# Kernel optimization log

Hardware: AMD Instinct MI355X
Metric: run time of the kernel (lower is better)

The kernel has to match this reference:

```python
import jax, jax.numpy as jnp
import numpy as np

N_NODES = 50000
N_EDGES = 800000
NFEAT = 128
NHID = 128
NCLASS = 10
NUM_GRAPHS = 512


def setup_inputs() -> dict:
    key = jax.random.key(0)
    ks = jax.random.split(key, 12)
    x = jax.random.normal(ks[0], (N_NODES, NFEAT), dtype=jnp.float32)
    edge_index = jax.random.randint(ks[1], (2, N_EDGES), 0, N_NODES, dtype=jnp.int64)
    batch = jnp.sort(jax.random.randint(ks[2], (N_NODES,), 0, NUM_GRAPHS, dtype=jnp.int64))
    def glorot(k, fan_in, fan_out):
        lim = np.sqrt(6.0 / (fan_in + fan_out))
        return jax.random.uniform(k, (fan_in, fan_out), jnp.float32, -lim, lim)
    return {
        "x": x, "edge_index": edge_index, "batch": batch,
        "W0": glorot(ks[3], NFEAT, NHID), "b0": jnp.zeros((NHID,), jnp.float32),
        "W1": glorot(ks[4], NHID, NHID), "b1": jnp.zeros((NHID,), jnp.float32),
        "W2": glorot(ks[5], NHID, NHID), "b2": jnp.zeros((NHID,), jnp.float32),
        "lin_w": glorot(ks[6], NHID, NCLASS), "lin_b": jnp.zeros((NCLASS,), jnp.float32),
    }


def _gcn_norm(edge_index, n):
    # PyG GCNConv: add self-loops, symmetric normalization D^-1/2 A D^-1/2
    loop = jnp.arange(n, dtype=edge_index.dtype)
    src = jnp.concatenate([edge_index[0], loop])  # [E+N]
    dst = jnp.concatenate([edge_index[1], loop])
    deg = jax.ops.segment_sum(jnp.ones_like(dst, dtype=jnp.float32), dst, num_segments=n)
    dis = jnp.where(deg > 0, jax.lax.rsqrt(jnp.maximum(deg, 1.0)), 0.0)
    norm = dis[src] * dis[dst]  # [E+N]
    return src, dst, norm


def _gcn_conv(x, W, b, src, dst, norm, n):
    h = x @ W                              # [N, nhid]
    msg = h[src] * norm[:, None]           # gather + scale, [E+N, nhid]
    out = jax.ops.segment_sum(msg, dst, num_segments=n)
    return out + b


def reference(x, edge_index, batch, W0, b0, W1, b1, W2, b2, lin_w, lin_b):
    n = x.shape[0]
    src, dst, norm = _gcn_norm(edge_index, n)
    h = x
    for (W, b) in ((W0, b0), (W1, b1), (W2, b2)):
        h = jax.nn.relu(_gcn_conv(h, W, b, src, dst, norm, n))
    # global mean pool over graphs
    sums = jax.ops.segment_sum(h, batch, num_segments=NUM_GRAPHS)
    cnts = jax.ops.segment_sum(jnp.ones((n,), jnp.float32), batch, num_segments=NUM_GRAPHS)
    pooled = sums / jnp.maximum(cnts, 1.0)[:, None]  # [G, nhid]
    logits = pooled @ lin_w + lin_b
    return jax.nn.log_softmax(logits, axis=-1)
```

## Files before the change

### kernel.cpp

```cpp
#include <hip/hip_runtime.h>
#include <hip/hip_fp16.h>


#define FEAT 128
#define NCLASS 10
#define NB_MAX 512

typedef _Float16 h8 __attribute__((ext_vector_type(8)));
typedef float f4 __attribute__((ext_vector_type(4)));

__device__ inline int swz(int row, int cbyte) { return row * 256 + (cbyte ^ ((row & 7) << 4)); }

__global__ void __launch_bounds__(256) hist_wt_kernel(const int* __restrict__ ei,
                                                      int* __restrict__ bhist,
                                                      int ne, int nb, int epb, int hb,
                                                      const float* __restrict__ W0,
                                                      const float* __restrict__ W1,
                                                      const float* __restrict__ W2,
                                                      _Float16* __restrict__ Wt) {
  int t = threadIdx.x;
  if (blockIdx.x >= hb) {
    int i = (blockIdx.x - hb) * 256 + t;
    if (i < 3 * FEAT * FEAT) {
      int l = i / (FEAT * FEAT);
      int r = i - l * (FEAT * FEAT);
      int nn = r >> 7, kk = r & 127;
      const float* W = (l == 0) ? W0 : (l == 1) ? W1 : W2;
      Wt[i] = (_Float16)W[kk * FEAT + nn];
    }
    return;
  }
  __shared__ int lh[NB_MAX];
  for (int i = t; i < nb; i += 256) lh[i] = 0;
  __syncthreads();
  int r0 = blockIdx.x * epb;
  int r1 = min(r0 + epb, ne);
  for (int k = r0 + t; k < r1; k += 256) atomicAdd(&lh[ei[ne + k] >> 7], 1);
  __syncthreads();
  for (int i = t; i < nb; i += 256)
    if (lh[i]) atomicAdd(&bhist[i], lh[i]);
}

__global__ void __launch_bounds__(512) bscan_kernel(const int* __restrict__ bhist,
                                                    int* __restrict__ bstart,
                                                    int* __restrict__ bcur,
                                                    int* __restrict__ off,
                                                    int nb, int n, int ne) {
  __shared__ int sh[512];
  int t = threadIdx.x;
  int v = (t < nb) ? bhist[t] : 0;
  sh[t] = v;
  __syncthreads();
  int x = v;
  for (int d = 1; d < 512; d <<= 1) {
    int y = (t >= d) ? sh[t - d] : 0;
    __syncthreads();
    x += y;
    sh[t] = x;
    __syncthreads();
  }
  if (t < nb) {
    bstart[t] = x - v;
    bcur[t] = x - v;
  }
  if (t == 0) {
    bstart[nb] = ne;
    off[n] = ne;
  }
}

__global__ void __launch_bounds__(256) scatter_kernel(const int* __restrict__ ei,
                                                      int* __restrict__ bcur,
                                                      unsigned* __restrict__ buf,
                                                      int ne, int nb, int epb) {
  __shared__ int lh[NB_MAX], lbs[NB_MAX];
  int t = threadIdx.x;
  for (int i = t; i < nb; i += 256) lh[i] = 0;
  __syncthreads();
  int r0 = blockIdx.x * epb;
  int r1 = min(r0 + epb, ne);
  for (int k = r0 + t; k < r1; k += 256) atomicAdd(&lh[ei[ne + k] >> 7], 1);
  __syncthreads();
  for (int i = t; i < nb; i += 256) {
    int c = lh[i];
    lbs[i] = c ? atomicAdd(&bcur[i], c) : 0;
    lh[i] = 0;
  }
  __syncthreads();
  for (int k = r0 + t; k < r1; k += 256) {
    int src = ei[k];
    int dst = ei[ne + k];
    int b = dst >> 7;
    int p = lbs[b] + atomicAdd(&lh[b], 1);
    buf[p] = (unsigned)src | ((unsigned)(dst & 127) << 25);
  }
}

__global__ void __launch_bounds__(256) bucket_build_kernel(const unsigned* __restrict__ buf,
                                                           const int* __restrict__ bstart,
                                                           int* __restrict__ off,
                                                           int* __restrict__ csr,
                                                           float* __restrict__ dis, int n) {
  __shared__ int cnt[128], cur[128], sh[128];
  int b = blockIdx.x, t = threadIdx.x;
  int e0 = bstart[b], e1 = bstart[b + 1];
  if (t < 128) cnt[t] = 0;
  __syncthreads();
  for (int k = e0 + t; k < e1; k += 256) atomicAdd(&cnt[buf[k] >> 25], 1);
  __syncthreads();
  int v = (t < 128) ? cnt[t] : 0;
  if (t < 128) sh[t] = v;
  __syncthreads();
  int x = v;
  for (int d = 1; d < 128; d <<= 1) {
    int y = (t < 128 && t >= d) ? sh[t - d] : 0;
    __syncthreads();
    if (t < 128) {
      x += y;
      sh[t] = x;
    }
    __syncthreads();
  }
  if (t < 128) {
    int node = (b << 7) + t;
    cur[t] = x - v;
    if (node < n) {
      off[node] = e0 + x - v;
      dis[node] = rsqrtf((float)(v + 1));
    }
  }
  __syncthreads();
  for (int k = e0 + t; k < e1; k += 256) {
    unsigned u = buf[k];
    int d = u >> 25;
    int p = atomicAdd(&cur[d], 1);
    csr[e0 + p] = (int)(u & 0x1FFFFFFu);
  }
}

template <bool F32IN>
__global__ void __launch_bounds__(256) gemm_mfma_kernel(const void* __restrict__ Xin,
                                                        const _Float16* __restrict__ Wt,
                                                        const float* __restrict__ dis,
                                                        _Float16* __restrict__ Hs, int n) {
  __shared__ _Float16 st[64 * FEAT];
  int tid = threadIdx.x;
  int w = tid >> 6, lane = tid & 63;
  int l15 = lane & 15, hi = lane >> 4;

  int rowA = blockIdx.x * 64 + w * 16 + l15;
  int rA = min(rowA, n - 1);
  const _Float16* Xh = (const _Float16*)Xin;
  const float* Xf = (const float*)Xin;

  f4 acc[8];
#pragma unroll
  for (int nb = 0; nb < 8; ++nb) acc[nb] = (f4)(0.f);

#pragma unroll
  for (int kk = 0; kk < FEAT; kk += 32) {
    int ko = kk + hi * 8;
    h8 a;
    if (F32IN) {
      float4 x0 = *(const float4*)&Xf[(size_t)rA * FEAT + ko];
      float4 x1 = *(const float4*)&Xf[(size_t)rA * FEAT + ko + 4];
      a[0] = (_Float16)x0.x; a[1] = (_Float16)x0.y; a[2] = (_Float16)x0.z; a[3] = (_Float16)x0.w;
      a[4] = (_Float16)x1.x; a[5] = (_Float16)x1.y; a[6] = (_Float16)x1.z; a[7] = (_Float16)x1.w;
    } else {
      a = *(const h8*)&Xh[(size_t)rA * FEAT + ko];
    }
#pragma unroll
    for (int nb = 0; nb < 8; ++nb) {
      h8 bfr = *(const h8*)&Wt[(nb * 16 + l15) * FEAT + ko];
      acc[nb] = __builtin_amdgcn_mfma_f32_16x16x32_f16(a, bfr, acc[nb], 0, 0, 0);
    }
  }

  float dv[4];
#pragma unroll
  for (int r = 0; r < 4; ++r) {
    int grow = blockIdx.x * 64 + w * 16 + hi * 4 + r;
    dv[r] = dis[min(grow, n - 1)];
  }
#pragma unroll
  for (int nb = 0; nb < 8; ++nb)
#pragma unroll
    for (int r = 0; r < 4; ++r)
      st[(w * 16 + hi * 4 + r) * FEAT + nb * 16 + l15] = (_Float16)(acc[nb][r] * dv[r]);
  __syncthreads();

  int rowbase = blockIdx.x * 64;
#pragma unroll
  for (int i = tid; i < 64 * FEAT / 8; i += 256) {
    int row = rowbase + (i >> 4);
    if (row < n)
      *(uint4*)&Hs[(size_t)row * FEAT + (i & 15) * 8] =
          *(const uint4*)&st[(i >> 4) * FEAT + (i & 15) * 8];
  }
}

__global__ void __launch_bounds__(256) fused_kernel(const h8* __restrict__ Hs_in,
                                                    const int* __restrict__ csr,
                                                    const int* __restrict__ off,
                                                    const float* __restrict__ dis,
                                                    const float* __restrict__ bias,
                                                    const _Float16* __restrict__ Wt,
                                                    _Float16* __restrict__ Hs_out, int n) {
  __shared__ char xsb[64 * 256];
  int tid = threadIdx.x;
  int w = tid >> 6, lane = tid & 63;
  int grp = lane >> 4, lig = lane & 15;
  int row0 = blockIdx.x * 64;
  int g16 = w * 4 + grp;

  float4 b0 = ((const float4*)bias)[lig * 2];
  float4 b1 = ((const float4*)bias)[lig * 2 + 1];
  float bb[8] = {b0.x, b0.y, b0.z, b0.w, b1.x, b1.y, b1.z, b1.w};

  for (int m = 0; m < 4; ++m) {
    int ar = g16 * 4 + m;
    int nd = min(row0 + ar, n - 1);
    int s = off[nd], e = off[nd + 1];
    float a0[8], a1[8], a2[8], a3[8];
    h8 v = Hs_in[(size_t)nd * 16 + lig];
#pragma unroll
    for (int j = 0; j < 8; ++j) {
      a0[j] = (float)v[j];
      a1[j] = a2[j] = a3[j] = 0.f;
    }
    for (int k = s; k < e; k += 4) {
      int i0 = csr[k];
      int i1 = (k + 1 < e) ? csr[k + 1] : -1;
      int i2 = (k + 2 < e) ? csr[k + 2] : -1;
      int i3 = (k + 3 < e) ? csr[k + 3] : -1;
      h8 v0 = Hs_in[(size_t)i0 * 16 + lig];
      h8 v1 = Hs_in[(size_t)max(i1, 0) * 16 + lig];
      h8 v2 = Hs_in[(size_t)max(i2, 0) * 16 + lig];
      h8 v3 = Hs_in[(size_t)max(i3, 0) * 16 + lig];
#pragma unroll
      for (int j = 0; j < 8; ++j) a0[j] += (float)v0[j];
      if (i1 >= 0) {
#pragma unroll
        for (int j = 0; j < 8; ++j) a1[j] += (float)v1[j];
      }
      if (i2 >= 0) {
#pragma unroll
        for (int j = 0; j < 8; ++j) a2[j] += (float)v2[j];
      }
      if (i3 >= 0) {
#pragma unroll
        for (int j = 0; j < 8; ++j) a3[j] += (float)v3[j];
      }
    }
    float d = dis[nd];
    h8 o;
#pragma unroll
    for (int j = 0; j < 8; ++j) {
      float sum = a0[j] + a1[j] + a2[j] + a3[j];
      o[j] = (_Float16)fmaxf(fmaf(d, sum, bb[j]), 0.f);
    }
    *(h8*)(xsb + swz(ar, lig * 16)) = o;
  }
  __syncthreads();

  int l15 = lane & 15, hi = lane >> 4;
  f4 acc[8];
#pragma unroll
  for (int nb = 0; nb < 8; ++nb) acc[nb] = (f4)(0.f);
#pragma unroll
  for (int kk = 0; kk < FEAT; kk += 32) {
    int ko = kk + hi * 8;
    h8 a = *(const h8*)(xsb + swz(w * 16 + l15, ko * 2));
#pragma unroll
    for (int nb = 0; nb < 8; ++nb) {
      h8 bfr = *(const h8*)&Wt[(nb * 16 + l15) * FEAT + ko];
      acc[nb] = __builtin_amdgcn_mfma_f32_16x16x32_f16(a, bfr, acc[nb], 0, 0, 0);
    }
  }

  float dv[4];
#pragma unroll
  for (int r = 0; r < 4; ++r) {
    int grow = row0 + w * 16 + hi * 4 + r;
    dv[r] = dis[min(grow, n - 1)];
  }
  __syncthreads();
#pragma unroll
  for (int nb = 0; nb < 8; ++nb)
#pragma unroll
    for (int r = 0; r < 4; ++r) {
      int srow = w * 16 + hi * 4 + r;
      *(_Float16*)(xsb + swz(srow, (nb * 16 + l15) * 2)) = (_Float16)(acc[nb][r] * dv[r]);
    }
  __syncthreads();
#pragma unroll
  for (int i = tid; i < 64 * FEAT / 8; i += 256) {
    int row = row0 + (i >> 4);
    if (row < n)
      *(uint4*)&Hs_out[(size_t)row * FEAT + (i & 15) * 8] =
          *(const uint4*)(xsb + swz(i >> 4, (i & 15) * 16));
  }
}

__global__ void __launch_bounds__(256) agg_kernel(const h8* __restrict__ Hs,
                                                  const int* __restrict__ csr,
                                                  const int* __restrict__ off,
                                                  const float* __restrict__ dis,
                                                  const float* __restrict__ b,
                                                  h8* __restrict__ out, int n) {
  int wave = threadIdx.x >> 6;
  int lane = threadIdx.x & 63;
  int grp = lane >> 4, lig = lane & 15;
  int node = blockIdx.x * 4 + wave;
  if (node >= n) return;
  int s = off[node];
  int e = off[node + 1];

  float acc[8];
  if (grp == 0) {
    h8 v = Hs[(size_t)node * 16 + lig];
#pragma unroll
    for (int j = 0; j < 8; ++j) acc[j] = (float)v[j];
  } else {
#pragma unroll
    for (int j = 0; j < 8; ++j) acc[j] = 0.f;
  }

  for (int k = s; k < e; k += 16) {
    int k0 = k + grp, k1 = k0 + 4, k2 = k0 + 8, k3 = k0 + 12;
    int i0 = (k0 < e) ? csr[k0] : -1;
    int i1 = (k1 < e) ? csr[k1] : -1;
    int i2 = (k2 < e) ? csr[k2] : -1;
    int i3 = (k3 < e) ? csr[k3] : -1;
    h8 v0 = Hs[(size_t)max(i0, 0) * 16 + lig];
    h8 v1 = Hs[(size_t)max(i1, 0) * 16 + lig];
    h8 v2 = Hs[(size_t)max(i2, 0) * 16 + lig];
    h8 v3 = Hs[(size_t)max(i3, 0) * 16 + lig];
    if (i0 >= 0) {
#pragma unroll
      for (int j = 0; j < 8; ++j) acc[j] += (float)v0[j];
    }
    if (i1 >= 0) {
#pragma unroll
      for (int j = 0; j < 8; ++j) acc[j] += (float)v1[j];
    }
    if (i2 >= 0) {
#pragma unroll
      for (int j = 0; j < 8; ++j) acc[j] += (float)v2[j];
    }
    if (i3 >= 0) {
#pragma unroll
      for (int j = 0; j < 8; ++j) acc[j] += (float)v3[j];
    }
  }

#pragma unroll
  for (int j = 0; j < 8; ++j) {
    acc[j] += __shfl_xor(acc[j], 16);
    acc[j] += __shfl_xor(acc[j], 32);
  }

  if (grp == 0) {
    float d = dis[node];
    float4 b0 = ((const float4*)b)[lig * 2];
    float4 b1 = ((const float4*)b)[lig * 2 + 1];
    h8 o;
    o[0] = (_Float16)fmaxf(fmaf(d, acc[0], b0.x), 0.f);
    o[1] = (_Float16)fmaxf(fmaf(d, acc[1], b0.y), 0.f);
    o[2] = (_Float16)fmaxf(fmaf(d, acc[2], b0.z), 0.f);
    o[3] = (_Float16)fmaxf(fmaf(d, acc[3], b0.w), 0.f);
    o[4] = (_Float16)fmaxf(fmaf(d, acc[4], b1.x), 0.f);
    o[5] = (_Float16)fmaxf(fmaf(d, acc[5], b1.y), 0.f);
    o[6] = (_Float16)fmaxf(fmaf(d, acc[6], b1.z), 0.f);
    o[7] = (_Float16)fmaxf(fmaf(d, acc[7], b1.w), 0.f);
    out[(size_t)node * 16 + lig] = o;
  }
}

__global__ void bounds_kernel(const int* __restrict__ batch, int* __restrict__ gstart,
                              int n, int g) {
  int i = blockIdx.x * 256 + threadIdx.x;
  if (i >= n) return;
  int bi = batch[i];
  int bp = (i == 0) ? -1 : batch[i - 1];
  for (int q = bp + 1; q <= bi; ++q) gstart[q] = i;
  if (i == n - 1) {
    for (int q = bi + 1; q <= g; ++q) gstart[q] = n;
  }
}

__global__ void __launch_bounds__(128) pool_kernel(const __half* __restrict__ h,
                                                   const int* __restrict__ gstart,
                                                   const float* __restrict__ lw,
                                                   const float* __restrict__ lb,
                                                   float* __restrict__ out) {
  int g = blockIdx.x;
  int t = threadIdx.x;
  int s = gstart[g];
  int e = gstart[g + 1];
  float a0 = 0.f, a1 = 0.f, a2 = 0.f, a3 = 0.f;
  int i = s;
  for (; i + 4 <= e; i += 4) {
    a0 += __half2float(h[(size_t)i * FEAT + t]);
    a1 += __half2float(h[(size_t)(i + 1) * FEAT + t]);
    a2 += __half2float(h[(size_t)(i + 2) * FEAT + t]);
    a3 += __half2float(h[(size_t)(i + 3) * FEAT + t]);
  }
  for (; i < e; ++i) a0 += __half2float(h[(size_t)i * FEAT + t]);
  float acc = a0 + a1 + a2 + a3;
  float cnt = (float)(e - s);
  float pooled = acc / fmaxf(cnt, 1.f);
  __shared__ float lds[FEAT];
  __shared__ float logits[NCLASS];
  lds[t] = pooled;
  __syncthreads();
  if (t < NCLASS) {
    float z = lb[t];
    for (int k = 0; k < FEAT; ++k) z += lds[k] * lw[k * NCLASS + t];
    logits[t] = z;
  }
  __syncthreads();
  if (t < NCLASS) {
    float m = logits[0];
#pragma unroll
    for (int c = 1; c < NCLASS; ++c) m = fmaxf(m, logits[c]);
    float ssum = 0.f;
#pragma unroll
    for (int c = 0; c < NCLASS; ++c) ssum += expf(logits[c] - m);
    out[(size_t)g * NCLASS + t] = logits[t] - m - logf(ssum);
  }
}

extern "C" void kernel_launch(void* const* d_in, const int* in_sizes, int n_in,
                              void* d_out, int out_size, void* d_ws, size_t ws_size,
                              hipStream_t stream) {
  const float* x = (const float*)d_in[0];
  const int* ei = (const int*)d_in[1];
  const int* batch = (const int*)d_in[2];
  const float* W0 = (const float*)d_in[3];
  const float* b0 = (const float*)d_in[4];
  const float* W1 = (const float*)d_in[5];
  const float* b1 = (const float*)d_in[6];
  const float* W2 = (const float*)d_in[7];
  const float* b2 = (const float*)d_in[8];
  const float* lw = (const float*)d_in[9];
  const float* lb = (const float*)d_in[10];

  int n = in_sizes[2];
  int ne = in_sizes[1] / 2;
  int g = out_size / NCLASS;
  int nb = (n + 127) >> 7;
  int hblocks = 120;
  int epb = (ne + hblocks - 1) / hblocks;
  int wtblocks = (3 * FEAT * FEAT + 255) / 256;

  char* ws = (char*)d_ws;
  size_t p = 0;
  auto alloc = [&](size_t bytes) {
    size_t cur = p;
    p += (bytes + 255) & ~(size_t)255;
    return cur;
  };
  int* off = (int*)(ws + alloc((size_t)(n + 1) * 4));
  int* csr = (int*)(ws + alloc((size_t)ne * 4));
  int* bhist = (int*)(ws + alloc((size_t)NB_MAX * 4));
  int* bstart = (int*)(ws + alloc((size_t)(NB_MAX + 1) * 4));
  int* bcur = (int*)(ws + alloc((size_t)NB_MAX * 4));
  int* gstart = (int*)(ws + alloc((size_t)(g + 1) * 4));
  float* dis = (float*)(ws + alloc((size_t)n * 4));
  unsigned* buf = (unsigned*)(ws + alloc((size_t)ne * 4));
  _Float16* Wt = (_Float16*)(ws + alloc((size_t)3 * FEAT * FEAT * 2));
  _Float16* HA = (_Float16*)(ws + alloc((size_t)n * FEAT * 2));
  _Float16* HB = (_Float16*)(ws + alloc((size_t)n * FEAT * 2));

  hipMemsetAsync(bhist, 0, NB_MAX * 4, stream);

  hist_wt_kernel<<<hblocks + wtblocks, 256, 0, stream>>>(ei, bhist, ne, nb, epb, hblocks,
                                                         W0, W1, W2, Wt);
  bscan_kernel<<<1, 512, 0, stream>>>(bhist, bstart, bcur, off, nb, n, ne);
  scatter_kernel<<<hblocks, 256, 0, stream>>>(ei, bcur, buf, ne, nb, epb);
  bucket_build_kernel<<<nb, 256, 0, stream>>>(buf, bstart, off, csr, dis, n);

  int gblocks = (n + 63) / 64;
  gemm_mfma_kernel<true><<<gblocks, 256, 0, stream>>>(x, Wt, dis, HA, n);
  fused_kernel<<<gblocks, 256, 0, stream>>>((const h8*)HA, csr, off, dis, b0,
                                            Wt + (size_t)1 * FEAT * FEAT, HB, n);
  fused_kernel<<<gblocks, 256, 0, stream>>>((const h8*)HB, csr, off, dis, b1,
                                            Wt + (size_t)2 * FEAT * FEAT, HA, n);
  agg_kernel<<<(n + 3) / 4, 256, 0, stream>>>((const h8*)HA, csr, off, dis, b2, (h8*)HB, n);

  bounds_kernel<<<(n + 255) / 256, 256, 0, stream>>>(batch, gstart, n, g);
  pool_kernel<<<g, 128, 0, stream>>>((const __half*)HB, gstart, lw, lb, (float*)d_out);
}
```

Before: 209.4 us.

## Fuse last aggregation with mean pooling and shrink fused blocks

The last GCN aggregation now pools directly into a per-graph float buffer. It accumulates in shared memory over the few graphs spanned by each 64-node block and falls back to global atomics for the rest, so the final layer no longer writes its full feature matrix and the pooling kernel no longer reads it back. The fused aggregate+GEMM kernel moves to 32-row, 128-thread blocks for more blocks in flight. The neighbor gather is unrolled to eight edges per iteration for more memory-level parallelism. In exchange this adds float atomics, which make the summation order nondeterministic, plus an extra memset.

```diff
diff --git a/kernel.cpp b/kernel.cpp
--- a/kernel.cpp
+++ b/kernel.cpp
@@ -5,11 +5,65 @@
 #define FEAT 128
 #define NCLASS 10
 #define NB_MAX 512
+#define GSPAN 8
 
 typedef _Float16 h8 __attribute__((ext_vector_type(8)));
 typedef float f4 __attribute__((ext_vector_type(4)));
 
 __device__ inline int swz(int row, int cbyte) { return row * 256 + (cbyte ^ ((row & 7) << 4)); }
+
+__device__ inline void gather8(const h8* __restrict__ Hs, const int* __restrict__ csr,
+                               int s, int e, int lig, float* a0, float* a1, float* a2,
+                               float* a3) {
+  for (int k = s; k < e; k += 8) {
+    int i0 = csr[k];
+    int i1 = (k + 1 < e) ? csr[k + 1] : -1;
+    int i2 = (k + 2 < e) ? csr[k + 2] : -1;
+    int i3 = (k + 3 < e) ? csr[k + 3] : -1;
+    int i4 = (k + 4 < e) ? csr[k + 4] : -1;
+    int i5 = (k + 5 < e) ? csr[k + 5] : -1;
+    int i6 = (k + 6 < e) ? csr[k + 6] : -1;
+    int i7 = (k + 7 < e) ? csr[k + 7] : -1;
+    h8 v0 = Hs[(size_t)i0 * 16 + lig];
+    h8 v1 = Hs[(size_t)max(i1, 0) * 16 + lig];
+    h8 v2 = Hs[(size_t)max(i2, 0) * 16 + lig];
+    h8 v3 = Hs[(size_t)max(i3, 0) * 16 + lig];
+    h8 v4 = Hs[(size_t)max(i4, 0) * 16 + lig];
+    h8 v5 = Hs[(size_t)max(i5, 0) * 16 + lig];
+    h8 v6 = Hs[(size_t)max(i6, 0) * 16 + lig];
+    h8 v7 = Hs[(size_t)max(i7, 0) * 16 + lig];
+#pragma unroll
+    for (int j = 0; j < 8; ++j) a0[j] += (float)v0[j];
+    if (i1 >= 0) {
+#pragma unroll
+      for (int j = 0; j < 8; ++j) a1[j] += (float)v1[j];
+    }
+    if (i2 >= 0) {
+#pragma unroll
+      for (int j = 0; j < 8; ++j) a2[j] += (float)v2[j];
+    }
+    if (i3 >= 0) {
+#pragma unroll
+      for (int j = 0; j < 8; ++j) a3[j] += (float)v3[j];
+    }
+    if (i4 >= 0) {
+#pragma unroll
+      for (int j = 0; j < 8; ++j) a0[j] += (float)v4[j];
+    }
+    if (i5 >= 0) {
+#pragma unroll
+      for (int j = 0; j < 8; ++j) a1[j] += (float)v5[j];
+    }
+    if (i6 >= 0) {
+#pragma unroll
+      for (int j = 0; j < 8; ++j) a2[j] += (float)v6[j];
+    }
+    if (i7 >= 0) {
+#pragma unroll
+      for (int j = 0; j < 8; ++j) a3[j] += (float)v7[j];
+    }
+  }
+}
 
 __global__ void __launch_bounds__(256) hist_wt_kernel(const int* __restrict__ ei,
                                                       int* __restrict__ bhist,
@@ -138,8 +192,7 @@
   }
 }
 
-template <bool F32IN>
-__global__ void __launch_bounds__(256) gemm_mfma_kernel(const void* __restrict__ Xin,
+__global__ void __launch_bounds__(256) gemm_mfma_kernel(const float* __restrict__ Xf,
                                                         const _Float16* __restrict__ Wt,
                                                         const float* __restrict__ dis,
                                                         _Float16* __restrict__ Hs, int n) {
@@ -150,8 +203,6 @@
 
   int rowA = blockIdx.x * 64 + w * 16 + l15;
   int rA = min(rowA, n - 1);
-  const _Float16* Xh = (const _Float16*)Xin;
-  const float* Xf = (const float*)Xin;
 
   f4 acc[8];
 #pragma unroll
@@ -161,14 +212,10 @@
   for (int kk = 0; kk < FEAT; kk += 32) {
     int ko = kk + hi * 8;
     h8 a;
-    if (F32IN) {
-      float4 x0 = *(const float4*)&Xf[(size_t)rA * FEAT + ko];
-      float4 x1 = *(const float4*)&Xf[(size_t)rA * FEAT + ko + 4];
-      a[0] = (_Float16)x0.x; a[1] = (_Float16)x0.y; a[2] = (_Float16)x0.z; a[3] = (_Float16)x0.w;
-      a[4] = (_Float16)x1.x; a[5] = (_Float16)x1.y; a[6] = (_Float16)x1.z; a[7] = (_Float16)x1.w;
-    } else {
-      a = *(const h8*)&Xh[(size_t)rA * FEAT + ko];
-    }
+    float4 x0 = *(const float4*)&Xf[(size_t)rA * FEAT + ko];
+    float4 x1 = *(const float4*)&Xf[(size_t)rA * FEAT + ko + 4];
+    a[0] = (_Float16)x0.x; a[1] = (_Float16)x0.y; a[2] = (_Float16)x0.z; a[3] = (_Float16)x0.w;
+    a[4] = (_Float16)x1.x; a[5] = (_Float16)x1.y; a[6] = (_Float16)x1.z; a[7] = (_Float16)x1.w;
 #pragma unroll
     for (int nb = 0; nb < 8; ++nb) {
       h8 bfr = *(const h8*)&Wt[(nb * 16 + l15) * FEAT + ko];
@@ -199,19 +246,17 @@
   }
 }
 
-__global__ void __launch_bounds__(256) fused_kernel(const h8* __restrict__ Hs_in,
+__global__ void __launch_bounds__(128) fused_kernel(const h8* __restrict__ Hs_in,
                                                     const int* __restrict__ csr,
                                                     const int* __restrict__ off,
                                                     const float* __restrict__ dis,
                                                     const float* __restrict__ bias,
                                                     const _Float16* __restrict__ Wt,
                                                     _Float16* __restrict__ Hs_out, int n) {
-  __shared__ char xsb[64 * 256];
+  __shared__ char xsb[32 * 256];
   int tid = threadIdx.x;
-  int w = tid >> 6, lane = tid & 63;
-  int grp = lane >> 4, lig = lane & 15;
-  int row0 = blockIdx.x * 64;
-  int g16 = w * 4 + grp;
+  int g16 = tid >> 4, lig = tid & 15;
+  int row0 = blockIdx.x * 32;
 
   float4 b0 = ((const float4*)bias)[lig * 2];
   float4 b1 = ((const float4*)bias)[lig * 2 + 1];
@@ -228,30 +273,7 @@
       a0[j] = (float)v[j];
       a1[j] = a2[j] = a3[j] = 0.f;
     }
-    for (int k = s; k < e; k += 4) {
-      int i0 = csr[k];
-      int i1 = (k + 1 < e) ? csr[k + 1] : -1;
-      int i2 = (k + 2 < e) ? csr[k + 2] : -1;
-      int i3 = (k + 3 < e) ? csr[k + 3] : -1;
-      h8 v0 = Hs_in[(size_t)i0 * 16 + lig];
-      h8 v1 = Hs_in[(size_t)max(i1, 0) * 16 + lig];
-      h8 v2 = Hs_in[(size_t)max(i2, 0) * 16 + lig];
-      h8 v3 = Hs_in[(size_t)max(i3, 0) * 16 + lig];
-#pragma unroll
-      for (int j = 0; j < 8; ++j) a0[j] += (float)v0[j];
-      if (i1 >= 0) {
-#pragma unroll
-        for (int j = 0; j < 8; ++j) a1[j] += (float)v1[j];
-      }
-      if (i2 >= 0) {
-#pragma unroll
-        for (int j = 0; j < 8; ++j) a2[j] += (float)v2[j];
-      }
-      if (i3 >= 0) {
-#pragma unroll
-        for (int j = 0; j < 8; ++j) a3[j] += (float)v3[j];
-      }
-    }
+    gather8(Hs_in, csr, s, e, lig, a0, a1, a2, a3);
     float d = dis[nd];
     h8 o;
 #pragma unroll
@@ -263,6 +285,7 @@
   }
   __syncthreads();
 
+  int w = tid >> 6, lane = tid & 63;
   int l15 = lane & 15, hi = lane >> 4;
   f4 acc[8];
 #pragma unroll
@@ -294,7 +317,7 @@
     }
   __syncthreads();
 #pragma unroll
-  for (int i = tid; i < 64 * FEAT / 8; i += 256) {
+  for (int i = tid; i < 32 * FEAT / 8; i += 128) {
     int row = row0 + (i >> 4);
     if (row < n)
       *(uint4*)&Hs_out[(size_t)row * FEAT + (i & 15) * 8] =
@@ -302,78 +325,62 @@
   }
 }
 
-__global__ void __launch_bounds__(256) agg_kernel(const h8* __restrict__ Hs,
-                                                  const int* __restrict__ csr,
-                                                  const int* __restrict__ off,
-                                                  const float* __restrict__ dis,
-                                                  const float* __restrict__ b,
-                                                  h8* __restrict__ out, int n) {
-  int wave = threadIdx.x >> 6;
-  int lane = threadIdx.x & 63;
-  int grp = lane >> 4, lig = lane & 15;
-  int node = blockIdx.x * 4 + wave;
-  if (node >= n) return;
-  int s = off[node];
-  int e = off[node + 1];
-
-  float acc[8];
-  if (grp == 0) {
+__global__ void __launch_bounds__(256) agg_pool_kernel(const h8* __restrict__ Hs,
+                                                       const int* __restrict__ csr,
+                                                       const int* __restrict__ off,
+                                                       const float* __restrict__ dis,
+                                                       const float* __restrict__ bias,
+                                                       const int* __restrict__ batch,
+                                                       float* __restrict__ pooled, int n) {
+  __shared__ float sums[GSPAN][FEAT];
+  int tid = threadIdx.x;
+  int g16 = tid >> 4, lig = tid & 15;
+  int row0 = blockIdx.x * 64;
+  int bmin = batch[min(row0, n - 1)];
+
+  for (int i = tid; i < GSPAN * FEAT; i += 256) sums[i >> 7][i & 127] = 0.f;
+  __syncthreads();
+
+  float4 b0 = ((const float4*)bias)[lig * 2];
+  float4 b1 = ((const float4*)bias)[lig * 2 + 1];
+  float bb[8] = {b0.x, b0.y, b0.z, b0.w, b1.x, b1.y, b1.z, b1.w};
+
+  for (int m = 0; m < 4; ++m) {
+    int node = row0 + g16 * 4 + m;
+    if (node >= n) break;
+    int s = off[node], e = off[node + 1];
+    float a0[8], a1[8], a2[8], a3[8];
     h8 v = Hs[(size_t)node * 16 + lig];
 #pragma unroll
-    for (int j = 0; j < 8; ++j) acc[j] = (float)v[j];
-  } else {
-#pragma unroll
-    for (int j = 0; j < 8; ++j) acc[j] = 0.f;
-  }
-
-  for (int k = s; k < e; k += 16) {
-    int k0 = k + grp, k1 = k0 + 4, k2 = k0 + 8, k3 = k0 + 12;
-    int i0 = (k0 < e) ? csr[k0] : -1;
-    int i1 = (k1 < e) ? csr[k1] : -1;
-    int i2 = (k2 < e) ? csr[k2] : -1;
-    int i3 = (k3 < e) ? csr[k3] : -1;
-    h8 v0 = Hs[(size_t)max(i0, 0) * 16 + lig];
-    h8 v1 = Hs[(size_t)max(i1, 0) * 16 + lig];
-    h8 v2 = Hs[(size_t)max(i2, 0) * 16 + lig];
-    h8 v3 = Hs[(size_t)max(i3, 0) * 16 + lig];
-    if (i0 >= 0) {
-#pragma unroll
-      for (int j = 0; j < 8; ++j) acc[j] += (float)v0[j];
-    }
-    if (i1 >= 0) {
-#pragma unroll
-      for (int j = 0; j < 8; ++j) acc[j] += (float)v1[j];
-    }
-    if (i2 >= 0) {
-#pragma unroll
-      for (int j = 0; j < 8; ++j) acc[j] += (float)v2[j];
-    }
-    if (i3 >= 0) {
-#pragma unroll
-      for (int j = 0; j < 8; ++j) acc[j] += (float)v3[j];
-    }
-  }
-
-#pragma unroll
-  for (int j = 0; j < 8; ++j) {
-    acc[j] += __shfl_xor(acc[j], 16);
-    acc[j] += __shfl_xor(acc[j], 32);
-  }
-
-  if (grp == 0) {
+    for (int j = 0; j < 8; ++j) {
+      a0[j] = (float)v[j];
+      a1[j] = a2[j] = a3[j] = 0.f;
+    }
+    gather8(Hs, csr, s, e, lig, a0, a1, a2, a3);
     float d = dis[node];
-    float4 b0 = ((const float4*)b)[lig * 2];
-    float4 b1 = ((const float4*)b)[lig * 2 + 1];
-    h8 o;
-    o[0] = (_Float16)fmaxf(fmaf(d, acc[0], b0.x), 0.f);
-    o[1] = (_Float16)fmaxf(fmaf(d, acc[1], b0.y), 0.f);
-    o[2] = (_Float16)fmaxf(fmaf(d, acc[2], b0.z), 0.f);
-    o[3] = (_Float16)fmaxf(fmaf(d, acc[3], b0.w), 0.f);
-    o[4] = (_Float16)fmaxf(fmaf(d, acc[4], b1.x), 0.f);
-    o[5] = (_Float16)fmaxf(fmaf(d, acc[5], b1.y), 0.f);
-    o[6] = (_Float16)fmaxf(fmaf(d, acc[6], b1.z), 0.f);
-    o[7] = (_Float16)fmaxf(fmaf(d, acc[7], b1.w), 0.f);
-    out[(size_t)node * 16 + lig] = o;
+    int gl = batch[node] - bmin;
+    if (gl < GSPAN) {
+#pragma unroll
+      for (int j = 0; j < 8; ++j) {
+        float sum = a0[j] + a1[j] + a2[j] + a3[j];
+        atomicAdd(&sums[gl][lig * 8 + j], fmaxf(fmaf(d, sum, bb[j]), 0.f));
+      }
+    } else {
+#pragma unroll
+      for (int j = 0; j < 8; ++j) {
+        float sum = a0[j] + a1[j] + a2[j] + a3[j];
+        atomicAdd(&pooled[(size_t)batch[node] * FEAT + lig * 8 + j],
+                  fmaxf(fmaf(d, sum, bb[j]), 0.f));
+      }
+    }
+  }
+  __syncthreads();
+
+  int bmax = batch[min(row0 + 63, n - 1)];
+  int span = min(bmax - bmin + 1, GSPAN);
+  for (int i = tid; i < span * FEAT; i += 256) {
+    float vv = sums[i >> 7][i & 127];
+    if (vv != 0.f) atomicAdd(&pooled[(size_t)(bmin + (i >> 7)) * FEAT + (i & 127)], vv);
   }
 }
 
@@ -389,30 +396,18 @@
   }
 }
 
-__global__ void __launch_bounds__(128) pool_kernel(const __half* __restrict__ h,
-                                                   const int* __restrict__ gstart,
-                                                   const float* __restrict__ lw,
-                                                   const float* __restrict__ lb,
-                                                   float* __restrict__ out) {
+__global__ void __launch_bounds__(128) pool2_kernel(const float* __restrict__ pooled,
+                                                    const int* __restrict__ gstart,
+                                                    const float* __restrict__ lw,
+                                                    const float* __restrict__ lb,
+                                                    float* __restrict__ out) {
   int g = blockIdx.x;
   int t = threadIdx.x;
-  int s = gstart[g];
-  int e = gstart[g + 1];
-  float a0 = 0.f, a1 = 0.f, a2 = 0.f, a3 = 0.f;
-  int i = s;
-  for (; i + 4 <= e; i += 4) {
-    a0 += __half2float(h[(size_t)i * FEAT + t]);
-    a1 += __half2float(h[(size_t)(i + 1) * FEAT + t]);
-    a2 += __half2float(h[(size_t)(i + 2) * FEAT + t]);
-    a3 += __half2float(h[(size_t)(i + 3) * FEAT + t]);
-  }
-  for (; i < e; ++i) a0 += __half2float(h[(size_t)i * FEAT + t]);
-  float acc = a0 + a1 + a2 + a3;
-  float cnt = (float)(e - s);
-  float pooled = acc / fmaxf(cnt, 1.f);
+  float cnt = (float)(gstart[g + 1] - gstart[g]);
+  float pv = pooled[(size_t)g * FEAT + t] / fmaxf(cnt, 1.f);
   __shared__ float lds[FEAT];
   __shared__ float logits[NCLASS];
-  lds[t] = pooled;
+  lds[t] = pv;
   __syncthreads();
   if (t < NCLASS) {
     float z = lb[t];
@@ -470,10 +465,12 @@
   float* dis = (float*)(ws + alloc((size_t)n * 4));
   unsigned* buf = (unsigned*)(ws + alloc((size_t)ne * 4));
   _Float16* Wt = (_Float16*)(ws + alloc((size_t)3 * FEAT * FEAT * 2));
+  float* pooled = (float*)(ws + alloc((size_t)g * FEAT * 4));
   _Float16* HA = (_Float16*)(ws + alloc((size_t)n * FEAT * 2));
   _Float16* HB = (_Float16*)(ws + alloc((size_t)n * FEAT * 2));
 
   hipMemsetAsync(bhist, 0, NB_MAX * 4, stream);
+  hipMemsetAsync(pooled, 0, (size_t)g * FEAT * 4, stream);
 
   hist_wt_kernel<<<hblocks + wtblocks, 256, 0, stream>>>(ei, bhist, ne, nb, epb, hblocks,
                                                          W0, W1, W2, Wt);
@@ -481,14 +478,14 @@
   scatter_kernel<<<hblocks, 256, 0, stream>>>(ei, bcur, buf, ne, nb, epb);
   bucket_build_kernel<<<nb, 256, 0, stream>>>(buf, bstart, off, csr, dis, n);
 
-  int gblocks = (n + 63) / 64;
-  gemm_mfma_kernel<true><<<gblocks, 256, 0, stream>>>(x, Wt, dis, HA, n);
-  fused_kernel<<<gblocks, 256, 0, stream>>>((const h8*)HA, csr, off, dis, b0,
-                                            Wt + (size_t)1 * FEAT * FEAT, HB, n);
-  fused_kernel<<<gblocks, 256, 0, stream>>>((const h8*)HB, csr, off, dis, b1,
-                                            Wt + (size_t)2 * FEAT * FEAT, HA, n);
-  agg_kernel<<<(n + 3) / 4, 256, 0, stream>>>((const h8*)HA, csr, off, dis, b2, (h8*)HB, n);
+  gemm_mfma_kernel<<<(n + 63) / 64, 256, 0, stream>>>(x, Wt, dis, HA, n);
+  fused_kernel<<<(n + 31) / 32, 128, 0, stream>>>((const h8*)HA, csr, off, dis, b0,
+                                                  Wt + (size_t)1 * FEAT * FEAT, HB, n);
+  fused_kernel<<<(n + 31) / 32, 128, 0, stream>>>((const h8*)HB, csr, off, dis, b1,
+                                                  Wt + (size_t)2 * FEAT * FEAT, HA, n);
+  agg_pool_kernel<<<(n + 63) / 64, 256, 0, stream>>>((const h8*)HA, csr, off, dis, b2,
+                                                     batch, pooled, n);
 
   bounds_kernel<<<(n + 255) / 256, 256, 0, stream>>>(batch, gstart, n, g);
-  pool_kernel<<<g, 128, 0, stream>>>((const __half*)HB, gstart, lw, lb, (float*)d_out);
-}
+  pool2_kernel<<<g, 128, 0, stream>>>(pooled, gstart, lw, lb, (float*)d_out);
+}
```

Result: slower. 238.4 us (+13.8%).

## Pad CSR rows to multiples of eight with a zero row, restructure aggregation

Applied to the files above, without the earlier changes.

Each node's neighbour list in the CSR is padded to a multiple of eight entries. The padding points at an extra zeroed feature row, and offsets are stored as (start,end) pairs. The gather loop can then run branch-free with vectorized int4 index loads and eight gathers in flight, replacing the guarded four-way loop. The final aggregation kernel now uses a 16-lanes-per-node layout with this gather, and the batch-bounds kernel is merged into the prep launch to remove one launch. The cost is extra CSR memory and wasted loads on the zero row for low-degree nodes.

```diff
diff --git a/kernel.cpp b/kernel.cpp
--- a/kernel.cpp
+++ b/kernel.cpp
@@ -11,14 +11,59 @@
 
 __device__ inline int swz(int row, int cbyte) { return row * 256 + (cbyte ^ ((row & 7) << 4)); }
 
-__global__ void __launch_bounds__(256) hist_wt_kernel(const int* __restrict__ ei,
-                                                      int* __restrict__ bhist,
-                                                      int ne, int nb, int epb, int hb,
-                                                      const float* __restrict__ W0,
-                                                      const float* __restrict__ W1,
-                                                      const float* __restrict__ W2,
-                                                      _Float16* __restrict__ Wt) {
+__device__ inline void gather_pad8(const h8* __restrict__ Hs, const int* __restrict__ csr,
+                                   int s, int e, int lig, float* a0, float* a1) {
+  int ep = s + ((e - s + 7) & ~7);
+  for (int k = s; k < ep; k += 8) {
+    int4 c0 = *(const int4*)&csr[k];
+    int4 c1 = *(const int4*)&csr[k + 4];
+    h8 v0 = Hs[(size_t)c0.x * 16 + lig];
+    h8 v1 = Hs[(size_t)c0.y * 16 + lig];
+    h8 v2 = Hs[(size_t)c0.z * 16 + lig];
+    h8 v3 = Hs[(size_t)c0.w * 16 + lig];
+    h8 v4 = Hs[(size_t)c1.x * 16 + lig];
+    h8 v5 = Hs[(size_t)c1.y * 16 + lig];
+    h8 v6 = Hs[(size_t)c1.z * 16 + lig];
+    h8 v7 = Hs[(size_t)c1.w * 16 + lig];
+#pragma unroll
+    for (int j = 0; j < 8; ++j) a0[j] += (float)v0[j];
+#pragma unroll
+    for (int j = 0; j < 8; ++j) a1[j] += (float)v1[j];
+#pragma unroll
+    for (int j = 0; j < 8; ++j) a0[j] += (float)v2[j];
+#pragma unroll
+    for (int j = 0; j < 8; ++j) a1[j] += (float)v3[j];
+#pragma unroll
+    for (int j = 0; j < 8; ++j) a0[j] += (float)v4[j];
+#pragma unroll
+    for (int j = 0; j < 8; ++j) a1[j] += (float)v5[j];
+#pragma unroll
+    for (int j = 0; j < 8; ++j) a0[j] += (float)v6[j];
+#pragma unroll
+    for (int j = 0; j < 8; ++j) a1[j] += (float)v7[j];
+  }
+}
+
+__global__ void __launch_bounds__(256) prep_kernel(const int* __restrict__ ei,
+                                                   int* __restrict__ bhist,
+                                                   int ne, int nb, int epb, int hb,
+                                                   const float* __restrict__ W0,
+                                                   const float* __restrict__ W1,
+                                                   const float* __restrict__ W2,
+                                                   _Float16* __restrict__ Wt, int wtb,
+                                                   const int* __restrict__ batch,
+                                                   int* __restrict__ gstart, int n, int g) {
   int t = threadIdx.x;
+  if (blockIdx.x >= hb + wtb) {
+    int i = (blockIdx.x - hb - wtb) * 256 + t;
+    if (i >= n) return;
+    int bi = batch[i];
+    int bp = (i == 0) ? -1 : batch[i - 1];
+    for (int q = bp + 1; q <= bi; ++q) gstart[q] = i;
+    if (i == n - 1)
+      for (int q = bi + 1; q <= g; ++q) gstart[q] = n;
+    return;
+  }
   if (blockIdx.x >= hb) {
     int i = (blockIdx.x - hb) * 256 + t;
     if (i < 3 * FEAT * FEAT) {
@@ -44,8 +89,7 @@
 __global__ void __launch_bounds__(512) bscan_kernel(const int* __restrict__ bhist,
                                                     int* __restrict__ bstart,
                                                     int* __restrict__ bcur,
-                                                    int* __restrict__ off,
-                                                    int nb, int n, int ne) {
+                                                    int nb, int ne) {
   __shared__ int sh[512];
   int t = threadIdx.x;
   int v = (t < nb) ? bhist[t] : 0;
@@ -63,10 +107,7 @@
     bstart[t] = x - v;
     bcur[t] = x - v;
   }
-  if (t == 0) {
-    bstart[nb] = ne;
-    off[n] = ne;
-  }
+  if (t == 0) bstart[nb] = ne;
 }
 
 __global__ void __launch_bounds__(256) scatter_kernel(const int* __restrict__ ei,
@@ -98,20 +139,25 @@
 
 __global__ void __launch_bounds__(256) bucket_build_kernel(const unsigned* __restrict__ buf,
                                                            const int* __restrict__ bstart,
-                                                           int* __restrict__ off,
+                                                           int2* __restrict__ offend,
                                                            int* __restrict__ csr,
                                                            float* __restrict__ dis, int n) {
-  __shared__ int cnt[128], cur[128], sh[128];
+  __shared__ int cnt[128], cur[128], sh[128], ps[128];
   int b = blockIdx.x, t = threadIdx.x;
   int e0 = bstart[b], e1 = bstart[b + 1];
+  int pb = ((e0 + 7) & ~7) + 1024 * b;
   if (t < 128) cnt[t] = 0;
   __syncthreads();
   for (int k = e0 + t; k < e1; k += 256) atomicAdd(&cnt[buf[k] >> 25], 1);
   __syncthreads();
-  int v = (t < 128) ? cnt[t] : 0;
-  if (t < 128) sh[t] = v;
-  __syncthreads();
-  int x = v;
+  int v = 0, pdv = 0;
+  if (t < 128) {
+    v = cnt[t];
+    pdv = (v + 7) & ~7;
+    sh[t] = pdv;
+  }
+  __syncthreads();
+  int x = pdv;
   for (int d = 1; d < 128; d <<= 1) {
     int y = (t < 128 && t >= d) ? sh[t - d] : 0;
     __syncthreads();
@@ -123,9 +169,11 @@
   }
   if (t < 128) {
     int node = (b << 7) + t;
-    cur[t] = x - v;
+    int st = x - pdv;
+    ps[t] = st;
+    cur[t] = st;
     if (node < n) {
-      off[node] = e0 + x - v;
+      offend[node] = make_int2(pb + st, pb + st + v);
       dis[node] = rsqrtf((float)(v + 1));
     }
   }
@@ -134,12 +182,16 @@
     unsigned u = buf[k];
     int d = u >> 25;
     int p = atomicAdd(&cur[d], 1);
-    csr[e0 + p] = (int)(u & 0x1FFFFFFu);
-  }
-}
-
-template <bool F32IN>
-__global__ void __launch_bounds__(256) gemm_mfma_kernel(const void* __restrict__ Xin,
+    csr[pb + p] = (int)(u & 0x1FFFFFFu);
+  }
+  __syncthreads();
+  if (t < 128) {
+    int pd = (cnt[t] + 7) & ~7;
+    for (int q = cnt[t]; q < pd; ++q) csr[pb + ps[t] + q] = n;
+  }
+}
+
+__global__ void __launch_bounds__(256) gemm_mfma_kernel(const float* __restrict__ Xf,
                                                         const _Float16* __restrict__ Wt,
                                                         const float* __restrict__ dis,
                                                         _Float16* __restrict__ Hs, int n) {
@@ -150,8 +202,6 @@
 
   int rowA = blockIdx.x * 64 + w * 16 + l15;
   int rA = min(rowA, n - 1);
-  const _Float16* Xh = (const _Float16*)Xin;
-  const float* Xf = (const float*)Xin;
 
   f4 acc[8];
 #pragma unroll
@@ -161,14 +211,10 @@
   for (int kk = 0; kk < FEAT; kk += 32) {
     int ko = kk + hi * 8;
     h8 a;
-    if (F32IN) {
-      float4 x0 = *(const float4*)&Xf[(size_t)rA * FEAT + ko];
-      float4 x1 = *(const float4*)&Xf[(size_t)rA * FEAT + ko + 4];
-      a[0] = (_Float16)x0.x; a[1] = (_Float16)x0.y; a[2] = (_Float16)x0.z; a[3] = (_Float16)x0.w;
-      a[4] = (_Float16)x1.x; a[5] = (_Float16)x1.y; a[6] = (_Float16)x1.z; a[7] = (_Float16)x1.w;
-    } else {
-      a = *(const h8*)&Xh[(size_t)rA * FEAT + ko];
-    }
+    float4 x0 = *(const float4*)&Xf[(size_t)rA * FEAT + ko];
+    float4 x1 = *(const float4*)&Xf[(size_t)rA * FEAT + ko + 4];
+    a[0] = (_Float16)x0.x; a[1] = (_Float16)x0.y; a[2] = (_Float16)x0.z; a[3] = (_Float16)x0.w;
+    a[4] = (_Float16)x1.x; a[5] = (_Float16)x1.y; a[6] = (_Float16)x1.z; a[7] = (_Float16)x1.w;
 #pragma unroll
     for (int nb = 0; nb < 8; ++nb) {
       h8 bfr = *(const h8*)&Wt[(nb * 16 + l15) * FEAT + ko];
@@ -201,7 +247,7 @@
 
 __global__ void __launch_bounds__(256) fused_kernel(const h8* __restrict__ Hs_in,
                                                     const int* __restrict__ csr,
-                                                    const int* __restrict__ off,
+                                                    const int2* __restrict__ offend,
                                                     const float* __restrict__ dis,
                                                     const float* __restrict__ bias,
                                                     const _Float16* __restrict__ Wt,
@@ -220,45 +266,20 @@
   for (int m = 0; m < 4; ++m) {
     int ar = g16 * 4 + m;
     int nd = min(row0 + ar, n - 1);
-    int s = off[nd], e = off[nd + 1];
-    float a0[8], a1[8], a2[8], a3[8];
+    int2 oe = offend[nd];
+    float a0[8], a1[8];
     h8 v = Hs_in[(size_t)nd * 16 + lig];
 #pragma unroll
     for (int j = 0; j < 8; ++j) {
       a0[j] = (float)v[j];
-      a1[j] = a2[j] = a3[j] = 0.f;
-    }
-    for (int k = s; k < e; k += 4) {
-      int i0 = csr[k];
-      int i1 = (k + 1 < e) ? csr[k + 1] : -1;
-      int i2 = (k + 2 < e) ? csr[k + 2] : -1;
-      int i3 = (k + 3 < e) ? csr[k + 3] : -1;
-      h8 v0 = Hs_in[(size_t)i0 * 16 + lig];
-      h8 v1 = Hs_in[(size_t)max(i1, 0) * 16 + lig];
-      h8 v2 = Hs_in[(size_t)max(i2, 0) * 16 + lig];
-      h8 v3 = Hs_in[(size_t)max(i3, 0) * 16 + lig];
-#pragma unroll
-      for (int j = 0; j < 8; ++j) a0[j] += (float)v0[j];
-      if (i1 >= 0) {
-#pragma unroll
-        for (int j = 0; j < 8; ++j) a1[j] += (float)v1[j];
-      }
-      if (i2 >= 0) {
-#pragma unroll
-        for (int j = 0; j < 8; ++j) a2[j] += (float)v2[j];
-      }
-      if (i3 >= 0) {
-#pragma unroll
-        for (int j = 0; j < 8; ++j) a3[j] += (float)v3[j];
-      }
-    }
+      a1[j] = 0.f;
+    }
+    gather_pad8(Hs_in, csr, oe.x, oe.y, lig, a0, a1);
     float d = dis[nd];
     h8 o;
 #pragma unroll
-    for (int j = 0; j < 8; ++j) {
-      float sum = a0[j] + a1[j] + a2[j] + a3[j];
-      o[j] = (_Float16)fmaxf(fmaf(d, sum, bb[j]), 0.f);
-    }
+    for (int j = 0; j < 8; ++j)
+      o[j] = (_Float16)fmaxf(fmaf(d, a0[j] + a1[j], bb[j]), 0.f);
     *(h8*)(xsb + swz(ar, lig * 16)) = o;
   }
   __syncthreads();
@@ -304,88 +325,36 @@
 
 __global__ void __launch_bounds__(256) agg_kernel(const h8* __restrict__ Hs,
                                                   const int* __restrict__ csr,
-                                                  const int* __restrict__ off,
+                                                  const int2* __restrict__ offend,
                                                   const float* __restrict__ dis,
-                                                  const float* __restrict__ b,
+                                                  const float* __restrict__ bias,
                                                   h8* __restrict__ out, int n) {
-  int wave = threadIdx.x >> 6;
-  int lane = threadIdx.x & 63;
-  int grp = lane >> 4, lig = lane & 15;
-  int node = blockIdx.x * 4 + wave;
-  if (node >= n) return;
-  int s = off[node];
-  int e = off[node + 1];
-
-  float acc[8];
-  if (grp == 0) {
+  int tid = threadIdx.x;
+  int g16 = tid >> 4, lig = tid & 15;
+  int row0 = blockIdx.x * 64;
+
+  float4 b0 = ((const float4*)bias)[lig * 2];
+  float4 b1 = ((const float4*)bias)[lig * 2 + 1];
+  float bb[8] = {b0.x, b0.y, b0.z, b0.w, b1.x, b1.y, b1.z, b1.w};
+
+  for (int m = 0; m < 4; ++m) {
+    int node = row0 + g16 * 4 + m;
+    if (node >= n) return;
+    int2 oe = offend[node];
+    float a0[8], a1[8];
     h8 v = Hs[(size_t)node * 16 + lig];
 #pragma unroll
-    for (int j = 0; j < 8; ++j) acc[j] = (float)v[j];
-  } else {
-#pragma unroll
-    for (int j = 0; j < 8; ++j) acc[j] = 0.f;
-  }
-
-  for (int k = s; k < e; k += 16) {
-    int k0 = k + grp, k1 = k0 + 4, k2 = k0 + 8, k3 = k0 + 12;
-    int i0 = (k0 < e) ? csr[k0] : -1;
-    int i1 = (k1 < e) ? csr[k1] : -1;
-    int i2 = (k2 < e) ? csr[k2] : -1;
-    int i3 = (k3 < e) ? csr[k3] : -1;
-    h8 v0 = Hs[(size_t)max(i0, 0) * 16 + lig];
-    h8 v1 = Hs[(size_t)max(i1, 0) * 16 + lig];
-    h8 v2 = Hs[(size_t)max(i2, 0) * 16 + lig];
-    h8 v3 = Hs[(size_t)max(i3, 0) * 16 + lig];
-    if (i0 >= 0) {
-#pragma unroll
-      for (int j = 0; j < 8; ++j) acc[j] += (float)v0[j];
-    }
-    if (i1 >= 0) {
-#pragma unroll
-      for (int j = 0; j < 8; ++j) acc[j] += (float)v1[j];
-    }
-    if (i2 >= 0) {
-#pragma unroll
-      for (int j = 0; j < 8; ++j) acc[j] += (float)v2[j];
-    }
-    if (i3 >= 0) {
-#pragma unroll
-      for (int j = 0; j < 8; ++j) acc[j] += (float)v3[j];
-    }
-  }
-
-#pragma unroll
-  for (int j = 0; j < 8; ++j) {
-    acc[j] += __shfl_xor(acc[j], 16);
-    acc[j] += __shfl_xor(acc[j], 32);
-  }
-
-  if (grp == 0) {
+    for (int j = 0; j < 8; ++j) {
+      a0[j] = (float)v[j];
+      a1[j] = 0.f;
+    }
+    gather_pad8(Hs, csr, oe.x, oe.y, lig, a0, a1);
     float d = dis[node];
-    float4 b0 = ((const float4*)b)[lig * 2];
-    float4 b1 = ((const float4*)b)[lig * 2 + 1];
     h8 o;
-    o[0] = (_Float16)fmaxf(fmaf(d, acc[0], b0.x), 0.f);
-    o[1] = (_Float16)fmaxf(fmaf(d, acc[1], b0.y), 0.f);
-    o[2] = (_Float16)fmaxf(fmaf(d, acc[2], b0.z), 0.f);
-    o[3] = (_Float16)fmaxf(fmaf(d, acc[3], b0.w), 0.f);
-    o[4] = (_Float16)fmaxf(fmaf(d, acc[4], b1.x), 0.f);
-    o[5] = (_Float16)fmaxf(fmaf(d, acc[5], b1.y), 0.f);
-    o[6] = (_Float16)fmaxf(fmaf(d, acc[6], b1.z), 0.f);
-    o[7] = (_Float16)fmaxf(fmaf(d, acc[7], b1.w), 0.f);
+#pragma unroll
+    for (int j = 0; j < 8; ++j)
+      o[j] = (_Float16)fmaxf(fmaf(d, a0[j] + a1[j], bb[j]), 0.f);
     out[(size_t)node * 16 + lig] = o;
-  }
-}
-
-__global__ void bounds_kernel(const int* __restrict__ batch, int* __restrict__ gstart,
-                              int n, int g) {
-  int i = blockIdx.x * 256 + threadIdx.x;
-  if (i >= n) return;
-  int bi = batch[i];
-  int bp = (i == 0) ? -1 : batch[i - 1];
-  for (int q = bp + 1; q <= bi; ++q) gstart[q] = i;
-  if (i == n - 1) {
-    for (int q = bi + 1; q <= g; ++q) gstart[q] = n;
   }
 }
 
@@ -453,6 +422,7 @@
   int hblocks = 120;
   int epb = (ne + hblocks - 1) / hblocks;
   int wtblocks = (3 * FEAT * FEAT + 255) / 256;
+  int bndblocks = (n + 255) / 256;
 
   char* ws = (char*)d_ws;
   size_t p = 0;
@@ -461,8 +431,8 @@
     p += (bytes + 255) & ~(size_t)255;
     return cur;
   };
-  int* off = (int*)(ws + alloc((size_t)(n + 1) * 4));
-  int* csr = (int*)(ws + alloc((size_t)ne * 4));
+  int2* offend = (int2*)(ws + alloc((size_t)n * 8));
+  int* csr = (int*)(ws + alloc(((size_t)ne + 1024 * nb + 64) * 4));
   int* bhist = (int*)(ws + alloc((size_t)NB_MAX * 4));
   int* bstart = (int*)(ws + alloc((size_t)(NB_MAX + 1) * 4));
   int* bcur = (int*)(ws + alloc((size_t)NB_MAX * 4));
@@ -470,25 +440,26 @@
   float* dis = (float*)(ws + alloc((size_t)n * 4));
   unsigned* buf = (unsigned*)(ws + alloc((size_t)ne * 4));
   _Float16* Wt = (_Float16*)(ws + alloc((size_t)3 * FEAT * FEAT * 2));
-  _Float16* HA = (_Float16*)(ws + alloc((size_t)n * FEAT * 2));
-  _Float16* HB = (_Float16*)(ws + alloc((size_t)n * FEAT * 2));
+  _Float16* HA = (_Float16*)(ws + alloc((size_t)(n + 1) * FEAT * 2));
+  _Float16* HB = (_Float16*)(ws + alloc((size_t)(n + 1) * FEAT * 2));
 
   hipMemsetAsync(bhist, 0, NB_MAX * 4, stream);
-
-  hist_wt_kernel<<<hblocks + wtblocks, 256, 0, stream>>>(ei, bhist, ne, nb, epb, hblocks,
-                                                         W0, W1, W2, Wt);
-  bscan_kernel<<<1, 512, 0, stream>>>(bhist, bstart, bcur, off, nb, n, ne);
+  hipMemsetAsync(HA + (size_t)n * FEAT, 0, FEAT * 2, stream);
+  hipMemsetAsync(HB + (size_t)n * FEAT, 0, FEAT * 2, stream);
+
+  prep_kernel<<<hblocks + wtblocks + bndblocks, 256, 0, stream>>>(
+      ei, bhist, ne, nb, epb, hblocks, W0, W1, W2, Wt, wtblocks, batch, gstart, n, g);
+  bscan_kernel<<<1, 512, 0, stream>>>(bhist, bstart, bcur, nb, ne);
   scatter_kernel<<<hblocks, 256, 0, stream>>>(ei, bcur, buf, ne, nb, epb);
-  bucket_build_kernel<<<nb, 256, 0, stream>>>(buf, bstart, off, csr, dis, n);
+  bucket_build_kernel<<<nb, 256, 0, stream>>>(buf, bstart, offend, csr, dis, n);
 
   int gblocks = (n + 63) / 64;
-  gemm_mfma_kernel<true><<<gblocks, 256, 0, stream>>>(x, Wt, dis, HA, n);
-  fused_kernel<<<gblocks, 256, 0, stream>>>((const h8*)HA, csr, off, dis, b0,
+  gemm_mfma_kernel<<<gblocks, 256, 0, stream>>>(x, Wt, dis, HA, n);
+  fused_kernel<<<gblocks, 256, 0, stream>>>((const h8*)HA, csr, offend, dis, b0,
                                             Wt + (size_t)1 * FEAT * FEAT, HB, n);
-  fused_kernel<<<gblocks, 256, 0, stream>>>((const h8*)HB, csr, off, dis, b1,
+  fused_kernel<<<gblocks, 256, 0, stream>>>((const h8*)HB, csr, offend, dis, b1,
                                             Wt + (size_t)2 * FEAT * FEAT, HA, n);
-  agg_kernel<<<(n + 3) / 4, 256, 0, stream>>>((const h8*)HA, csr, off, dis, b2, (h8*)HB, n);
-
-  bounds_kernel<<<(n + 255) / 256, 256, 0, stream>>>(batch, gstart, n, g);
+  agg_kernel<<<gblocks, 256, 0, stream>>>((const h8*)HA, csr, offend, dis, b2, (h8*)HB, n);
+
   pool_kernel<<<g, 128, 0, stream>>>((const __half*)HB, gstart, lw, lb, (float*)d_out);
 }
```

Measured after the change: 225.4 us. 1.08x slower.
